# Kernel optimization log

Measured on AMD Instinct MI355X. Metric: run time of the kernel, lower is better.

## Reference

```python
import jax, jax.numpy as jnp
import numpy as np

N, E, D, OUT = 50000, 800000, 64, 64
NEG_INF = jnp.float32(-1e30)


def _masked_edge_softmax(logits, mask, dst, n):
    # softmax over incoming edges of each dst node, restricted to mask
    l = jnp.where(mask, logits, NEG_INF)
    m = jax.ops.segment_max(l, dst, num_segments=n)        # [N]
    m = jnp.maximum(m, NEG_INF)                            # empty segments -> -1e30
    e = jnp.where(mask, jnp.exp(l - m[dst]), jnp.float32(0.0))  # [E]
    s = jax.ops.segment_sum(e, dst, num_segments=n)        # [N]
    return e / (s[dst] + jnp.float32(1e-16))               # [E]


def setup_inputs() -> dict:
    key = jax.random.key(0)
    ks = jax.random.split(key, 6)
    feat = jax.random.normal(ks[0], (N, D), dtype=jnp.float32)
    w = jax.random.normal(ks[1], (E,), dtype=jnp.float32)
    src = jax.random.randint(ks[2], (E,), 0, N, dtype=jnp.int32)
    dst = jax.random.randint(ks[3], (E,), 0, N, dtype=jnp.int32)
    # xavier_uniform with relu gain on fc weight
    gain = np.sqrt(2.0)
    limit = np.float32(gain * np.sqrt(6.0 / (3 * D + OUT)))
    W_fc = jax.random.uniform(ks[4], (OUT, 3 * D), jnp.float32, -limit, limit)
    b_fc = jnp.zeros((OUT,), jnp.float32)
    bias = jnp.zeros((OUT,), jnp.float32)
    return {
        "feat": feat, "w": w, "W_fc": W_fc, "b_fc": b_fc, "bias": bias,
        "coef_self": jnp.ones((1,), jnp.float32),
        "coef_posi": jnp.ones((1,), jnp.float32),
        "coef_nega": jnp.ones((1,), jnp.float32),
        "src": src, "dst": dst,
    }


def reference(feat, w, W_fc, b_fc, bias, coef_self, coef_posi, coef_nega, src, dst):
    n = feat.shape[0]
    pos_mask = w > 0
    neg_mask = w < 0
    # edge softmax over signed subgraphs (negative subgraph uses |w|)
    a_pos = _masked_edge_softmax(w, pos_mask, dst, n)              # [E]
    a_neg = _masked_edge_softmax(jnp.abs(w), neg_mask, dst, n)     # [E]
    # u_mul_e -> sum aggregation: gather source feats, weight, scatter to dst
    src_feat = feat[src]                                           # [E, D]
    h_pos = jax.ops.segment_sum(src_feat * a_pos[:, None], dst, num_segments=n)
    h_neg = jax.ops.segment_sum(src_feat * a_neg[:, None], dst, num_segments=n)
    feat_combined = jnp.concatenate(
        [coef_self * feat, coef_posi * h_pos, coef_nega * h_neg], axis=1)  # [N, 3D]
    rst = feat_combined @ W_fc.T + b_fc + bias
    return rst
```

## Files before the change

kernel.cpp:

```cpp
#include <hip/hip_runtime.h>

#define D 64
#define K3 192
#define OUTD 64
#define KPB 512
#define KPB_LOG 9
#define NBMAX 256
#define ABATCH 4096
#define CAP 8192

typedef __attribute__((ext_vector_type(8))) short bf16x8;
typedef __attribute__((ext_vector_type(4))) float f32x4;

static __device__ __forceinline__ unsigned short f2bf(float f) {
    unsigned u = __float_as_uint(f);
    u += 0x7fffu + ((u >> 16) & 1u);
    return (unsigned short)(u >> 16);
}
static __device__ __forceinline__ float bf2f(unsigned short h) {
    return __uint_as_float((unsigned)h << 16);
}

__global__ __launch_bounds__(256) void prep_kernel(
        const float* __restrict__ W_fc,
        const float* __restrict__ coef_self,
        const float* __restrict__ coef_posi,
        const float* __restrict__ coef_nega,
        const float* __restrict__ feat,
        unsigned short* __restrict__ Bfrag,
        unsigned short* __restrict__ feat16,
        int* __restrict__ cursorA, int NB, int ND4) {
    int i = blockIdx.x * blockDim.x + threadIdx.x;
    if (i < NB) cursorA[i] = i * CAP;
    if (i < 6 * 4 * 64 * 8) {
        int j    = i & 7;
        int lane = (i >> 3) & 63;
        int nt   = (i >> 9) & 3;
        int kt   = i >> 11;
        int n = nt * 16 + (lane & 15);
        int k = kt * 32 + (lane >> 4) * 8 + j;
        float cf = (k < 64) ? coef_self[0] : (k < 128 ? coef_posi[0] : coef_nega[0]);
        Bfrag[i] = f2bf(W_fc[n * K3 + k] * cf);
    }
    if (i < ND4) {
        float4 v = *(const float4*)&feat[(size_t)i * 4];
        unsigned long long p =
            (unsigned long long)f2bf(v.x) |
            ((unsigned long long)f2bf(v.y) << 16) |
            ((unsigned long long)f2bf(v.z) << 32) |
            ((unsigned long long)f2bf(v.w) << 48);
        *(unsigned long long*)&feat16[(size_t)i * 4] = p;
    }
}

__global__ __launch_bounds__(256) void bin_kernel(
        const float* __restrict__ w, const int* __restrict__ src,
        const int* __restrict__ dst, int* __restrict__ cursorA,
        uint2* __restrict__ staged, int E, int NB) {
    __shared__ int cnt[NBMAX];
    __shared__ int base[NBMAX];
    int t = threadIdx.x;
    int e0 = blockIdx.x * ABATCH;
    for (int i = t; i < NB; i += 256) cnt[i] = 0;
    __syncthreads();

    unsigned wv[16], yv[16];
    int bk[16], rk[16];
#pragma unroll
    for (int j = 0; j < 16; ++j) {
        int e = e0 + j * 256 + t;
        if (e < E) {
            float we = w[e];
            int key = 2 * dst[e] + (we < 0.0f ? 1 : 0);
            wv[j] = __float_as_uint(we);
            yv[j] = ((unsigned)src[e] << KPB_LOG) | (unsigned)(key & (KPB - 1));
            bk[j] = key >> KPB_LOG;
            rk[j] = atomicAdd(&cnt[bk[j]], 1);
        } else {
            bk[j] = -1;
        }
    }
    __syncthreads();
    for (int b = t; b < NB; b += 256) {
        int c = cnt[b];
        if (c > 0) base[b] = atomicAdd(&cursorA[b], c);
    }
    __syncthreads();
#pragma unroll
    for (int j = 0; j < 16; ++j) {
        if (bk[j] >= 0) {
            int pos = base[bk[j]] + rk[j];
            if (pos < (bk[j] + 1) * CAP)
                staged[pos] = make_uint2(wv[j], yv[j]);
        }
    }
}

__global__ __launch_bounds__(256) void bucket_scatter_kernel(
        const int* __restrict__ cursorA, const uint2* __restrict__ staged,
        int2* __restrict__ seg_be, uint2* __restrict__ e_pack, int M) {
    __shared__ int cnt[KPB];
    __shared__ int wt[4];
    int b = blockIdx.x;
    int t = threadIdx.x;
    int lane = t & 63;
    int wid = t >> 6;
    int kb = b << KPB_LOG;
    int nk = min(KPB, M - kb);
    int beg = b * CAP;
    int end = min(cursorA[b], beg + CAP);

    cnt[2 * t] = 0;
    cnt[2 * t + 1] = 0;
    __syncthreads();
    for (int i = beg + t; i < end; i += 256)
        atomicAdd(&cnt[staged[i].y & (KPB - 1)], 1);
    __syncthreads();

    int v0 = cnt[2 * t], v1 = cnt[2 * t + 1];
    int ps = v0 + v1;
    int incl = ps;
#pragma unroll
    for (int o = 1; o < 64; o <<= 1) {
        int u = __shfl_up(incl, o);
        if (lane >= o) incl += u;
    }
    if (lane == 63) wt[wid] = incl;
    __syncthreads();
    int wb = 0;
    for (int j = 0; j < wid; ++j) wb += wt[j];
    int excl = wb + (incl - ps);

    int p0 = beg + excl;
    int p1 = p0 + v0;
    if (2 * t < nk) seg_be[kb + 2 * t] = make_int2(p0, p1);
    if (2 * t + 1 < nk) seg_be[kb + 2 * t + 1] = make_int2(p1, p1 + v1);
    __syncthreads();
    cnt[2 * t] = p0;
    cnt[2 * t + 1] = p1;
    __syncthreads();

    for (int i = beg + t; i < end; i += 256) {
        uint2 r = staged[i];
        int kl = (int)(r.y & (KPB - 1));
        int p = atomicAdd(&cnt[kl], 1);
        e_pack[p] = make_uint2(r.x, r.y >> KPB_LOG);
    }
}

__global__ __launch_bounds__(256) void node_agg_kernel(
        const unsigned short* __restrict__ feat16,
        const int2* __restrict__ seg_be,
        const uint2* __restrict__ e_pack,
        unsigned short* __restrict__ h_pos,
        unsigned short* __restrict__ h_neg, int N) {
    int lane = threadIdx.x & 63;
    int seg = (blockIdx.x * blockDim.x + threadIdx.x) >> 6;
    if (seg >= 2 * N) return;
    int2 be = seg_be[seg];
    int beg = __builtin_amdgcn_readfirstlane(be.x);
    int end = __builtin_amdgcn_readfirstlane(be.y);
    int isneg = seg & 1;

    float s = 0.0f, acc = 0.0f;
    if (isneg) {
#pragma unroll 4
        for (int e = beg; e < end; ++e) {
            uint2 pk = e_pack[e];
            float ws = __uint_as_float(pk.x);
            float aj = __expf(-ws);
            s += aj;
            float fv = bf2f(feat16[(size_t)(int)pk.y * D + lane]);
            acc = fmaf(fv, aj, acc);
        }
    } else {
#pragma unroll 4
        for (int e = beg; e < end; ++e) {
            uint2 pk = e_pack[e];
            float ws = __uint_as_float(pk.x);
            float aj = (ws > 0.0f) ? __expf(ws) : 0.0f;
            s += aj;
            float fv = bf2f(feat16[(size_t)(int)pk.y * D + lane]);
            acc = fmaf(fv, aj, acc);
        }
    }
    float r = acc / (s + 1e-16f);
    unsigned short* h = isneg ? h_neg : h_pos;
    h[(size_t)(seg >> 1) * D + lane] = f2bf(r);
}

__global__ __launch_bounds__(256) void out_gemm_mfma(
        const unsigned short* __restrict__ feat16,
        const unsigned short* __restrict__ h_pos,
        const unsigned short* __restrict__ h_neg,
        const unsigned short* __restrict__ Bfrag,
        const float* __restrict__ b_fc,
        const float* __restrict__ bias,
        float* __restrict__ out,
        int N) {
    int lane = threadIdx.x & 63;
    int wv = (blockIdx.x * blockDim.x + threadIdx.x) >> 6;
    int node0 = wv * 16;
    if (node0 >= N) return;

    const bf16x8* bp = (const bf16x8*)Bfrag;
    bf16x8 bfr[24];
#pragma unroll
    for (int f = 0; f < 24; ++f) bfr[f] = bp[f * 64 + lane];

    const unsigned short* segs[3];
    segs[0] = feat16;
    segs[1] = h_pos;
    segs[2] = h_neg;

    int m = lane & 15;
    int kg = lane >> 4;
    int node = node0 + m;
    bool mvalid = node < N;

    f32x4 acc[4];
#pragma unroll
    for (int nt = 0; nt < 4; ++nt) acc[nt] = (f32x4){0.f, 0.f, 0.f, 0.f};

#pragma unroll
    for (int kt = 0; kt < 6; ++kt) {
        int sg = kt >> 1;
        bf16x8 a;
        if (mvalid) {
            a = *(const bf16x8*)(segs[sg] + (size_t)node * D + (kt & 1) * 32 + kg * 8);
        } else {
            a = (bf16x8){0, 0, 0, 0, 0, 0, 0, 0};
        }
#pragma unroll
        for (int nt = 0; nt < 4; ++nt)
            acc[nt] = __builtin_amdgcn_mfma_f32_16x16x32_bf16(
                a, bfr[kt * 4 + nt], acc[nt], 0, 0, 0);
    }

#pragma unroll
    for (int nt = 0; nt < 4; ++nt) {
        int col = nt * 16 + m;
        float bb = b_fc[col] + bias[col];
#pragma unroll
        for (int j = 0; j < 4; ++j) {
            int row = node0 + 4 * kg + j;
            if (row < N) out[(size_t)row * OUTD + col] = acc[nt][j] + bb;
        }
    }
}

extern "C" void kernel_launch(void* const* d_in, const int* in_sizes, int n_in,
                              void* d_out, int out_size, void* d_ws, size_t ws_size,
                              hipStream_t stream) {
    const float* feat      = (const float*)d_in[0];
    const float* w         = (const float*)d_in[1];
    const float* W_fc      = (const float*)d_in[2];
    const float* b_fc      = (const float*)d_in[3];
    const float* bias      = (const float*)d_in[4];
    const float* coef_self = (const float*)d_in[5];
    const float* coef_posi = (const float*)d_in[6];
    const float* coef_nega = (const float*)d_in[7];
    const int*   src       = (const int*)d_in[8];
    const int*   dst       = (const int*)d_in[9];

    const int E = in_sizes[1];
    const int N = in_sizes[0] / D;
    const int M = 2 * N;
    const int NB = (M + KPB - 1) / KPB;

    char* ws = (char*)d_ws;
    int2*  seg_be   = (int2*)ws;
    int*   cursorA  = (int*)(ws + (size_t)M * 8);
    size_t bfrag_off = (((size_t)M * 8 + (size_t)NB * 4) + 15) & ~(size_t)15;
    unsigned short* Bfrag = (unsigned short*)(ws + bfrag_off);
    size_t feat16_off = bfrag_off + 6 * 4 * 64 * 8 * 2;
    unsigned short* feat16 = (unsigned short*)(ws + feat16_off);
    size_t epack_off = (feat16_off + (size_t)N * D * 2 + 7) & ~(size_t)7;
    uint2* e_pack  = (uint2*)(ws + epack_off);
    uint2* staged  = e_pack + (size_t)NB * CAP;
    unsigned short* h_pos = (unsigned short*)((char*)(staged + (size_t)NB * CAP));
    unsigned short* h_neg = h_pos + (size_t)N * D;

    const int ND4 = N * D / 4;
    int pb = (max(ND4, 6 * 4 * 64 * 8) + 255) / 256;
    prep_kernel<<<pb, 256, 0, stream>>>(W_fc, coef_self, coef_posi, coef_nega,
                                        feat, Bfrag, feat16, cursorA, NB, ND4);
    bin_kernel<<<(E + ABATCH - 1) / ABATCH, 256, 0, stream>>>(
        w, src, dst, cursorA, staged, E, NB);
    bucket_scatter_kernel<<<NB, 256, 0, stream>>>(cursorA, staged, seg_be,
                                                  e_pack, M);

    int segb = (M * 64 + 255) / 256;
    node_agg_kernel<<<segb, 256, 0, stream>>>(feat16, seg_be, e_pack,
                                              h_pos, h_neg, N);

    int nwaves = (N + 15) / 16;
    int gb = (nwaves + 3) / 4;
    out_gemm_mfma<<<gb, 256, 0, stream>>>(feat16, h_pos, h_neg, Bfrag,
                                          b_fc, bias, (float*)d_out, N);
}
```

Baseline: 84.78 us.

## Fuse node aggregation and output GEMM via LDS-staged h tiles

Merges the per-segment softmax aggregation kernel and the MFMA output GEMM into one kernel. Each 512-thread block aggregates 128 segments (64 nodes, pos and neg) into padded shared memory, then runs the MFMA GEMM, with each wave computing half the output columns. This removes the h_pos/h_neg global round trip and one launch. In exchange, each wave now processes 16 segments serially, which may reduce latency hiding and lengthen the tail on high-degree nodes, and the block-wide barrier can leave waves idle.

```diff
diff --git a/kernel.cpp b/kernel.cpp
--- a/kernel.cpp
+++ b/kernel.cpp
@@ -8,6 +8,8 @@
 #define NBMAX 256
 #define ABATCH 4096
 #define CAP 8192
+#define NPB 64
+#define HSTRIDE 72
 
 typedef __attribute__((ext_vector_type(8))) short bf16x8;
 typedef __attribute__((ext_vector_type(4))) float f32x4;
@@ -148,103 +150,99 @@
     }
 }
 
-__global__ __launch_bounds__(256) void node_agg_kernel(
+__global__ __launch_bounds__(512) void agg_gemm_kernel(
         const unsigned short* __restrict__ feat16,
         const int2* __restrict__ seg_be,
         const uint2* __restrict__ e_pack,
-        unsigned short* __restrict__ h_pos,
-        unsigned short* __restrict__ h_neg, int N) {
-    int lane = threadIdx.x & 63;
-    int seg = (blockIdx.x * blockDim.x + threadIdx.x) >> 6;
-    if (seg >= 2 * N) return;
-    int2 be = seg_be[seg];
-    int beg = __builtin_amdgcn_readfirstlane(be.x);
-    int end = __builtin_amdgcn_readfirstlane(be.y);
-    int isneg = seg & 1;
-
-    float s = 0.0f, acc = 0.0f;
-    if (isneg) {
-#pragma unroll 4
-        for (int e = beg; e < end; ++e) {
-            uint2 pk = e_pack[e];
-            float ws = __uint_as_float(pk.x);
-            float aj = __expf(-ws);
-            s += aj;
-            float fv = bf2f(feat16[(size_t)(int)pk.y * D + lane]);
-            acc = fmaf(fv, aj, acc);
-        }
-    } else {
-#pragma unroll 4
-        for (int e = beg; e < end; ++e) {
-            uint2 pk = e_pack[e];
-            float ws = __uint_as_float(pk.x);
-            float aj = (ws > 0.0f) ? __expf(ws) : 0.0f;
-            s += aj;
-            float fv = bf2f(feat16[(size_t)(int)pk.y * D + lane]);
-            acc = fmaf(fv, aj, acc);
-        }
-    }
-    float r = acc / (s + 1e-16f);
-    unsigned short* h = isneg ? h_neg : h_pos;
-    h[(size_t)(seg >> 1) * D + lane] = f2bf(r);
-}
-
-__global__ __launch_bounds__(256) void out_gemm_mfma(
-        const unsigned short* __restrict__ feat16,
-        const unsigned short* __restrict__ h_pos,
-        const unsigned short* __restrict__ h_neg,
         const unsigned short* __restrict__ Bfrag,
         const float* __restrict__ b_fc,
         const float* __restrict__ bias,
         float* __restrict__ out,
         int N) {
-    int lane = threadIdx.x & 63;
-    int wv = (blockIdx.x * blockDim.x + threadIdx.x) >> 6;
-    int node0 = wv * 16;
-    if (node0 >= N) return;
-
+    __shared__ __align__(16) unsigned short h_lds[128 * HSTRIDE];
+    int t = threadIdx.x;
+    int lane = t & 63;
+    int wv = t >> 6;
+    int node0 = blockIdx.x * NPB;
+    int M = 2 * N;
+
+    int ch = wv & 1;
     const bf16x8* bp = (const bf16x8*)Bfrag;
-    bf16x8 bfr[24];
-#pragma unroll
-    for (int f = 0; f < 24; ++f) bfr[f] = bp[f * 64 + lane];
-
-    const unsigned short* segs[3];
-    segs[0] = feat16;
-    segs[1] = h_pos;
-    segs[2] = h_neg;
-
+    bf16x8 bfr[12];
+#pragma unroll
+    for (int kt = 0; kt < 6; ++kt)
+#pragma unroll
+        for (int x = 0; x < 2; ++x)
+            bfr[kt * 2 + x] = bp[(kt * 4 + 2 * ch + x) * 64 + lane];
+
+    for (int q = 0; q < 16; ++q) {
+        int sl = wv * 16 + q;
+        int seg = node0 * 2 + sl;
+        if (seg >= M) break;
+        int2 be = seg_be[seg];
+        int beg = __builtin_amdgcn_readfirstlane(be.x);
+        int end = __builtin_amdgcn_readfirstlane(be.y);
+        float s = 0.0f, acc = 0.0f;
+        if (seg & 1) {
+#pragma unroll 4
+            for (int e = beg; e < end; ++e) {
+                uint2 pk = e_pack[e];
+                float wsv = __uint_as_float(pk.x);
+                float aj = __expf(-wsv);
+                s += aj;
+                acc = fmaf(bf2f(feat16[(size_t)(int)pk.y * D + lane]), aj, acc);
+            }
+        } else {
+#pragma unroll 4
+            for (int e = beg; e < end; ++e) {
+                uint2 pk = e_pack[e];
+                float wsv = __uint_as_float(pk.x);
+                float aj = (wsv > 0.0f) ? __expf(wsv) : 0.0f;
+                s += aj;
+                acc = fmaf(bf2f(feat16[(size_t)(int)pk.y * D + lane]), aj, acc);
+            }
+        }
+        h_lds[sl * HSTRIDE + lane] = f2bf(acc / (s + 1e-16f));
+    }
+    __syncthreads();
+
+    int ng = wv >> 1;
     int m = lane & 15;
     int kg = lane >> 4;
-    int node = node0 + m;
+    int node = node0 + ng * 16 + m;
     bool mvalid = node < N;
-
-    f32x4 acc[4];
-#pragma unroll
-    for (int nt = 0; nt < 4; ++nt) acc[nt] = (f32x4){0.f, 0.f, 0.f, 0.f};
+    int ln2 = (ng * 16 + m) * 2;
+
+    f32x4 acc2[2];
+    acc2[0] = (f32x4){0.f, 0.f, 0.f, 0.f};
+    acc2[1] = (f32x4){0.f, 0.f, 0.f, 0.f};
 
 #pragma unroll
     for (int kt = 0; kt < 6; ++kt) {
         int sg = kt >> 1;
         bf16x8 a;
-        if (mvalid) {
-            a = *(const bf16x8*)(segs[sg] + (size_t)node * D + (kt & 1) * 32 + kg * 8);
+        if (sg == 0) {
+            if (mvalid)
+                a = *(const bf16x8*)(feat16 + (size_t)node * D + (kt & 1) * 32 + kg * 8);
+            else
+                a = (bf16x8){0, 0, 0, 0, 0, 0, 0, 0};
         } else {
-            a = (bf16x8){0, 0, 0, 0, 0, 0, 0, 0};
-        }
-#pragma unroll
-        for (int nt = 0; nt < 4; ++nt)
-            acc[nt] = __builtin_amdgcn_mfma_f32_16x16x32_bf16(
-                a, bfr[kt * 4 + nt], acc[nt], 0, 0, 0);
-    }
-
-#pragma unroll
-    for (int nt = 0; nt < 4; ++nt) {
-        int col = nt * 16 + m;
+            a = *(const bf16x8*)&h_lds[(ln2 + (sg - 1)) * HSTRIDE + (kt & 1) * 32 + kg * 8];
+        }
+#pragma unroll
+        for (int x = 0; x < 2; ++x)
+            acc2[x] = __builtin_amdgcn_mfma_f32_16x16x32_bf16(
+                a, bfr[kt * 2 + x], acc2[x], 0, 0, 0);
+    }
+
+#pragma unroll
+    for (int x = 0; x < 2; ++x) {
+        int col = (2 * ch + x) * 16 + m;
         float bb = b_fc[col] + bias[col];
 #pragma unroll
         for (int j = 0; j < 4; ++j) {
-            int row = node0 + 4 * kg + j;
-            if (row < N) out[(size_t)row * OUTD + col] = acc[nt][j] + bb;
+            int row = node0 + ng * 16 + 4 * kg + j;
+            if (row < N) out[(size_t)row * OUTD + col] = acc2[x][j] + bb;
         }
     }
 }
@@ -278,8 +276,6 @@
     size_t epack_off = (feat16_off + (size_t)N * D * 2 + 7) & ~(size_t)7;
     uint2* e_pack  = (uint2*)(ws + epack_off);
     uint2* staged  = e_pack + (size_t)NB * CAP;
-    unsigned short* h_pos = (unsigned short*)((char*)(staged + (size_t)NB * CAP));
-    unsigned short* h_neg = h_pos + (size_t)N * D;
 
     const int ND4 = N * D / 4;
     int pb = (max(ND4, 6 * 4 * 64 * 8) + 255) / 256;
@@ -290,12 +286,7 @@
     bucket_scatter_kernel<<<NB, 256, 0, stream>>>(cursorA, staged, seg_be,
                                                   e_pack, M);
 
-    int segb = (M * 64 + 255) / 256;
-    node_agg_kernel<<<segb, 256, 0, stream>>>(feat16, seg_be, e_pack,
-                                              h_pos, h_neg, N);
-
-    int nwaves = (N + 15) / 16;
-    int gb = (nwaves + 3) / 4;
-    out_gemm_mfma<<<gb, 256, 0, stream>>>(feat16, h_pos, h_neg, Bfrag,
-                                          b_fc, bias, (float*)d_out, N);
-}
+    int gb = (N + NPB - 1) / NPB;
+    agg_gemm_kernel<<<gb, 512, 0, stream>>>(feat16, seg_be, e_pack, Bfrag,
+                                            b_fc, bias, (float*)d_out, N);
+}
```

After: 104.5 us, median of 4. 23.2% more time.

## Precompute edge exp weights in scatter and aggregate four segments per wave

Applied to the files above, without the earlier changes.

The exponential of each edge weight now happens once in the bucket scatter pass and is stored in the packed edge record, so the aggregation loop only loads a ready coefficient. The aggregation kernel now assigns two nodes, four segments in all (pos and neg for each), to each wave. It runs their edge chains interleaved up to the longest length, which gives four independent gather chains for more memory-level parallelism. In exchange, masked iterations are wasted on the shorter segments, and the exp work moves into the scatter kernel.

```diff
diff --git a/kernel.cpp b/kernel.cpp
--- a/kernel.cpp
+++ b/kernel.cpp
@@ -143,8 +143,11 @@
     for (int i = beg + t; i < end; i += 256) {
         uint2 r = staged[i];
         int kl = (int)(r.y & (KPB - 1));
+        float wv = __uint_as_float(r.x);
+        float a = (kl & 1) ? __expf(-wv)
+                           : ((wv > 0.0f) ? __expf(wv) : 0.0f);
         int p = atomicAdd(&cnt[kl], 1);
-        e_pack[p] = make_uint2(r.x, r.y >> KPB_LOG);
+        e_pack[p] = make_uint2(__float_as_uint(a), r.y >> KPB_LOG);
     }
 }
 
@@ -155,38 +158,53 @@
         unsigned short* __restrict__ h_pos,
         unsigned short* __restrict__ h_neg, int N) {
     int lane = threadIdx.x & 63;
-    int seg = (blockIdx.x * blockDim.x + threadIdx.x) >> 6;
-    if (seg >= 2 * N) return;
-    int2 be = seg_be[seg];
-    int beg = __builtin_amdgcn_readfirstlane(be.x);
-    int end = __builtin_amdgcn_readfirstlane(be.y);
-    int isneg = seg & 1;
-
-    float s = 0.0f, acc = 0.0f;
-    if (isneg) {
-#pragma unroll 4
-        for (int e = beg; e < end; ++e) {
-            uint2 pk = e_pack[e];
-            float ws = __uint_as_float(pk.x);
-            float aj = __expf(-ws);
-            s += aj;
-            float fv = bf2f(feat16[(size_t)(int)pk.y * D + lane]);
-            acc = fmaf(fv, aj, acc);
-        }
-    } else {
-#pragma unroll 4
-        for (int e = beg; e < end; ++e) {
-            uint2 pk = e_pack[e];
-            float ws = __uint_as_float(pk.x);
-            float aj = (ws > 0.0f) ? __expf(ws) : 0.0f;
-            s += aj;
-            float fv = bf2f(feat16[(size_t)(int)pk.y * D + lane]);
-            acc = fmaf(fv, aj, acc);
-        }
-    }
-    float r = acc / (s + 1e-16f);
-    unsigned short* h = isneg ? h_neg : h_pos;
-    h[(size_t)(seg >> 1) * D + lane] = f2bf(r);
+    int pr = (blockIdx.x * blockDim.x + threadIdx.x) >> 6;
+    int n0 = 2 * pr;
+    if (n0 >= N) return;
+    const int4* be4 = (const int4*)&seg_be[2 * n0];
+    int4 beA = be4[0];
+    int eP0 = __builtin_amdgcn_readfirstlane(beA.x);
+    int dP0 = __builtin_amdgcn_readfirstlane(beA.y);
+    int eN0 = __builtin_amdgcn_readfirstlane(beA.z);
+    int dN0 = __builtin_amdgcn_readfirstlane(beA.w);
+    int eP1 = 0, dP1 = 0, eN1 = 0, dN1 = 0;
+    bool has1 = (n0 + 1) < N;
+    if (has1) {
+        int4 beB = be4[1];
+        eP1 = __builtin_amdgcn_readfirstlane(beB.x);
+        dP1 = __builtin_amdgcn_readfirstlane(beB.y);
+        eN1 = __builtin_amdgcn_readfirstlane(beB.z);
+        dN1 = __builtin_amdgcn_readfirstlane(beB.w);
+    }
+
+    float sP0 = 0.f, aP0 = 0.f, sN0 = 0.f, aN0 = 0.f;
+    float sP1 = 0.f, aP1 = 0.f, sN1 = 0.f, aN1 = 0.f;
+
+    int len = max(max(dP0 - eP0, dN0 - eN0), max(dP1 - eP1, dN1 - eN1));
+#define CHAIN(eB, dB, sAcc, vAcc)                                            \
+    {                                                                        \
+        int e = eB + i;                                                      \
+        bool v = e < dB;                                                     \
+        uint2 pk = e_pack[v ? e : 0];                 \
+        float a = v ? __uint_as_float(pk.x) : 0.0f;                          \
+        sAcc += a;                                                           \
+        vAcc = fmaf(bf2f(feat16[(size_t)(int)pk.y * D + lane]), a, vAcc);    \
+    }
+#pragma unroll 2
+    for (int i = 0; i < len; ++i) {
+        CHAIN(eP0, dP0, sP0, aP0)
+        CHAIN(eN0, dN0, sN0, aN0)
+        CHAIN(eP1, dP1, sP1, aP1)
+        CHAIN(eN1, dN1, sN1, aN1)
+    }
+#undef CHAIN
+
+    h_pos[(size_t)n0 * D + lane] = f2bf(aP0 / (sP0 + 1e-16f));
+    h_neg[(size_t)n0 * D + lane] = f2bf(aN0 / (sN0 + 1e-16f));
+    if (has1) {
+        h_pos[(size_t)(n0 + 1) * D + lane] = f2bf(aP1 / (sP1 + 1e-16f));
+        h_neg[(size_t)(n0 + 1) * D + lane] = f2bf(aN1 / (sN1 + 1e-16f));
+    }
 }
 
 __global__ __launch_bounds__(256) void out_gemm_mfma(
@@ -290,9 +308,10 @@
     bucket_scatter_kernel<<<NB, 256, 0, stream>>>(cursorA, staged, seg_be,
                                                   e_pack, M);
 
-    int segb = (M * 64 + 255) / 256;
-    node_agg_kernel<<<segb, 256, 0, stream>>>(feat16, seg_be, e_pack,
-                                              h_pos, h_neg, N);
+    int npairs = (N + 1) / 2;
+    int nodeb = (npairs * 64 + 255) / 256;
+    node_agg_kernel<<<nodeb, 256, 0, stream>>>(feat16, seg_be, e_pack,
+                                               h_pos, h_neg, N);
 
     int nwaves = (N + 15) / 16;
     int gb = (nwaves + 3) / 4;
```

After: 98.81 us. +16.6%, slower.
